# Kernel optimization log

Measured on AMD Instinct MI355X. Metric: run time of the kernel, lower is better.

The kernel has to match this reference:

```python
import jax, jax.numpy as jnp
import numpy as np

N = 1024
ODE_UNFOLDS = 6
EPS = 1e-8
RICCATI_ITERS = 6  # fixed-point DARE iteration standing in for the (undefined) lqr() helper
MASK_DENSITY = 0.4


def lqr(A, B, Q, R):
    # Discrete-time Riccati iteration: P <- A'PA - A'PB (R+B'PB)^{-1} B'PA + Q
    P = Q
    for _ in range(RICCATI_ITERS):
        BtP = B.T @ P                         # [N,N]
        K = jnp.linalg.solve(R + BtP @ B, BtP @ A)
        P = A.T @ P @ (A - B @ K) + Q
    BtP = B.T @ P
    K = jnp.linalg.solve(R + BtP @ B, BtP @ A)
    return K, P


def setup_inputs() -> dict:
    key = jax.random.key(0)
    ks = jax.random.split(key, 24)
    u = lambda k, shape, lo, hi: jax.random.uniform(k, shape, jnp.float32, lo, hi)
    # sprandsym-style SPD laplacian param, rescaled to [0.001, 1]
    rng = np.random.default_rng(0)
    X = (rng.standard_normal((N, N)) * (rng.random((N, N)) < 0.1)).astype(np.float32)
    A = X @ X.T + 0.01 * np.eye(N, dtype=np.float32)
    A = (A - A.min()) / (A.max() - A.min())
    lap = (A * (1.0 - 0.001) + 0.001).astype(np.float32)

    mask = (jax.random.uniform(ks[2], (N, N)) < MASK_DENSITY).astype(jnp.float32)
    smask = (jax.random.uniform(ks[3], (N, N)) < MASK_DENSITY).astype(jnp.float32)
    return dict(
        inputs=jax.random.normal(ks[0], (N,), jnp.float32),
        adj=jax.random.uniform(ks[1], (N, N), jnp.float32) / N,  # scaled for numerical stability of the Riccati loop
        laplacian=jnp.asarray(lap),
        control=u(ks[6], (N,), 0.001, 4.0),
        gleak=u(ks[7], (N,), 0.001, 1.0),
        vleak=u(ks[8], (N,), -0.2, 0.2),
        cm=u(ks[9], (N,), 0.4, 0.6),
        sigma=u(ks[10], (N, N), 3.0, 8.0),
        mu=u(ks[11], (N, N), 0.3, 0.8),
        w=u(ks[12], (N, N), 0.001, 1.0),
        erev=jnp.sign(jax.random.normal(ks[4], (N, N))) * mask,
        sensory_sigma=u(ks[13], (N, N), 3.0, 8.0),
        sensory_mu=u(ks[14], (N, N), 0.3, 0.8),
        sensory_w=u(ks[15], (N, N), 0.001, 1.0),
        sensory_erev=jnp.sign(jax.random.normal(ks[5], (N, N))) * smask,
        sparsity_mask=mask,
        sensory_sparsity_mask=smask,
        input_w=jnp.ones((N,), jnp.float32),
        input_b=jnp.zeros((N,), jnp.float32),
        output_w=jnp.ones((N,), jnp.float32),
        output_b=jnp.zeros((N,), jnp.float32),
        attn_w=jax.random.normal(ks[16], (N,), jnp.float32) / jnp.sqrt(N),
        attn_b=jax.random.normal(ks[17], (1,), jnp.float32),
        gc_w=jax.random.normal(ks[18], (1, 1), jnp.float32),
        gc_b=jax.random.normal(ks[19], (1,), jnp.float32),
    )


def reference(inputs, adj, laplacian, control, gleak, vleak, cm, sigma, mu, w, erev,
              sensory_sigma, sensory_mu, sensory_w, sensory_erev,
              sparsity_mask, sensory_sparsity_mask,
              input_w, input_b, output_w, output_b, attn_w, attn_b, gc_w, gc_b):
    x = inputs * input_w + input_b                      # _map_inputs (affine)
    n = x.shape[0]

    # ControlAttention with R = Q = eye(N): fc(I) rows = attn_w + attn_b
    att = attn_w + attn_b[0]                            # [N]
    s = x * att
    att_e = jnp.exp(s - jnp.max(s))                     # stable exp weighting
    Qm = jnp.diag(att_e)
    Rm = jnp.diag(att_e)                                # Q_att == R_att since Q == R == I

    K, _ = lqr(adj, laplacian, Qm, Rm)                  # K: [N,N]
    ctrl = (control - jnp.mean(K * x, axis=1)) @ laplacian  # [N]

    # sensory synapse activation (constant over the unfold loop)
    sens_act = sensory_w * jax.nn.sigmoid(sensory_sigma * (x[:, None] - sensory_mu)) * sensory_sparsity_mask
    w_num_s = jnp.sum(sens_act * sensory_erev, axis=1)  # [N]
    w_den_s = jnp.sum(sens_act, axis=1)                 # [N]

    gcn = lambda h: jax.nn.relu(adj @ (h * gc_w[0, 0]) + gc_b[0])
    d = x[:, None]
    for _ in range(4):
        d = gcn(d)
    d = d[:, 0]

    cm_t = d + cm * ODE_UNFOLDS + ctrl                  # elapsed_time = 1.0 -> cm / (1/unfolds)

    v = jnp.zeros((n,), x.dtype)                        # states default: zeros
    for _ in range(ODE_UNFOLDS):
        w_act = w * jax.nn.sigmoid(sigma * (v[:, None] - mu)) * sparsity_mask
        w_num = jnp.sum(w_act * erev, axis=1) + w_num_s
        w_den = jnp.sum(w_act, axis=1) + w_den_s
        v = (cm_t * v + gleak * vleak + w_num) / (cm_t + gleak + w_den + EPS)

    out = v * output_w + output_b                       # motor_size == state_size path
    return out, v, laplacian, ctrl + control
```

## Files before the change

### kernel.cpp

```cpp
#include <hip/hip_runtime.h>

#define MSZ (1024*1024)
#define LD 1024


__global__ __launch_bounds__(1024) void prep_k(const float* __restrict__ inp, const float* __restrict__ iw,
    const float* __restrict__ ib, const float* __restrict__ aw, const float* __restrict__ ab,
    float* __restrict__ xv, float* __restrict__ atte) {
  __shared__ float red[1024];
  int t = threadIdx.x;
  float x = inp[t] * iw[t] + ib[t];
  float s = x * (aw[t] + ab[0]);
  xv[t] = x;
  red[t] = s;
  __syncthreads();
  for (int o = 512; o > 0; o >>= 1) { if (t < o) red[t] = fmaxf(red[t], red[t + o]); __syncthreads(); }
  atte[t] = expf(s - red[0]);
}

__global__ void setdiag_k(float* __restrict__ P, const float* __restrict__ atte) {
  int idx = blockIdx.x * 256 + threadIdx.x;
  int r = idx >> 10, c = idx & 1023;
  P[idx] = (r == c) ? atte[r] : 0.0f;
}

__global__ __launch_bounds__(256) void sens_k(const float* __restrict__ sw, const float* __restrict__ ssig,
    const float* __restrict__ smu, const float* __restrict__ serev, const float* __restrict__ smask,
    const float* __restrict__ xv, float* __restrict__ wns, float* __restrict__ wds) {
  __shared__ float rn[256], rd[256];
  int i = blockIdx.x, t = threadIdx.x;
  float xi = xv[i];
  float n = 0.f, d = 0.f;
  for (int j = t; j < 1024; j += 256) {
    int idx = i * 1024 + j;
    float z = ssig[idx] * (xi - smu[idx]);
    float sg = 1.0f / (1.0f + expf(-z));
    float act = sw[idx] * sg * smask[idx];
    n += act * serev[idx];
    d += act;
  }
  rn[t] = n; rd[t] = d;
  __syncthreads();
  for (int o = 128; o > 0; o >>= 1) { if (t < o) { rn[t] += rn[t + o]; rd[t] += rd[t + o]; } __syncthreads(); }
  if (t == 0) { wns[i] = rn[0]; wds[i] = rd[0]; }
}

__global__ __launch_bounds__(256) void gcn_k(const float* __restrict__ adj, const float* __restrict__ hin,
    float* __restrict__ hout, const float* __restrict__ gcw, const float* __restrict__ gcb) {
  __shared__ float red[256];
  int i = blockIdx.x, t = threadIdx.x;
  float s = 0.f;
  for (int j = t; j < 1024; j += 256) s += adj[(size_t)i * 1024 + j] * hin[j];
  red[t] = s; __syncthreads();
  for (int o = 128; o > 0; o >>= 1) { if (t < o) red[t] += red[t + o]; __syncthreads(); }
  if (t == 0) hout[i] = fmaxf(gcw[0] * red[0] + gcb[0], 0.0f);
}

__global__ __launch_bounds__(256) void matvec_n_k(const float* __restrict__ M, const float* __restrict__ v,
    float* __restrict__ out) {
  __shared__ float red[256];
  int i = blockIdx.x, t = threadIdx.x;
  float s = 0.f;
  for (int j = t; j < 1024; j += 256) s += M[(size_t)i * 1024 + j] * v[j];
  red[t] = s; __syncthreads();
  for (int o = 128; o > 0; o >>= 1) { if (t < o) red[t] += red[t + o]; __syncthreads(); }
  if (t == 0) out[i] = red[0];
}

__global__ __launch_bounds__(256) void matvec_t_k(const float* __restrict__ M, const float* __restrict__ v,
    float* __restrict__ out) {
  int j = blockIdx.x * 256 + threadIdx.x;
  float s = 0.f;
  for (int i = 0; i < 1024; i++) s += M[(size_t)i * 1024 + j] * v[i];
  out[j] = s;
}

__global__ void gctrl_k(const float* __restrict__ control, const float* __restrict__ u, float* __restrict__ g) {
  int t = blockIdx.x * 256 + threadIdx.x;
  g[t] = control[t] - u[t] * (1.0f / 1024.0f);
}

__global__ void copylap_k(const float4* __restrict__ src, float4* __restrict__ dst) {
  int i = blockIdx.x * 256 + threadIdx.x;
  dst[i] = src[i];
}


struct GDesc { const float* A; const float* B; float* C; const float* diag; int tri; int mode; };
struct GArgs { GDesc d[3]; };

template<int TA>
__global__ __launch_bounds__(256) void gemm64x128_k(GArgs ga) {
  GDesc de = ga.d[blockIdx.z];
  int row0 = blockIdx.y * 64, col0 = blockIdx.x * 128;
  if (de.tri && row0 + 64 <= col0) return;
  __shared__ float As[32][64];
  __shared__ float Bs[32][128];
  const float* __restrict__ A = de.A;
  const float* __restrict__ B = de.B;
  int t = threadIdx.x;
  int tx = t & 15, ty = t >> 4;
  float acc[4][8] = {};
  for (int k0 = 0; k0 < 1024; k0 += 32) {
    if (TA == 1) {
      #pragma unroll
      for (int h = 0; h < 2; h++) {
        int s = h * 256 + t;
        int bk = s >> 4, am = (s & 15) * 4;
        float4 v = *(const float4*)(A + (size_t)(k0 + bk) * LD + row0 + am);
        *(float4*)(&As[bk][am]) = v;
      }
    } else {
      #pragma unroll
      for (int h = 0; h < 2; h++) {
        int s = h * 256 + t;
        int am = s >> 3, k4 = (s & 7) * 4;
        float4 v = *(const float4*)(A + (size_t)(row0 + am) * LD + k0 + k4);
        As[k4 + 0][am] = v.x; As[k4 + 1][am] = v.y; As[k4 + 2][am] = v.z; As[k4 + 3][am] = v.w;
      }
    }
    #pragma unroll
    for (int h = 0; h < 4; h++) {
      int s = h * 256 + t;
      int bk = s >> 5, bn = (s & 31) * 4;
      float4 v = *(const float4*)(B + (size_t)(k0 + bk) * LD + col0 + bn);
      *(float4*)(&Bs[bk][bn]) = v;
    }
    __syncthreads();
    #pragma unroll
    for (int k = 0; k < 32; k++) {
      float4 a4 = *(float4*)(&As[k][tx * 4]);
      float4 b0 = *(float4*)(&Bs[k][ty * 8]);
      float4 b1 = *(float4*)(&Bs[k][ty * 8 + 4]);
      float a[4] = {a4.x, a4.y, a4.z, a4.w};
      float b[8] = {b0.x, b0.y, b0.z, b0.w, b1.x, b1.y, b1.z, b1.w};
      #pragma unroll
      for (int i = 0; i < 4; i++)
        #pragma unroll
        for (int j = 0; j < 8; j++)
          acc[i][j] += a[i] * b[j];
    }
    __syncthreads();
  }
  #pragma unroll
  for (int i = 0; i < 4; i++) {
    int gm = row0 + tx * 4 + i;
    if (de.diag) {
      int dc = gm - col0 - ty * 8;
      if (dc >= 0 && dc < 8) acc[i][dc] += de.diag[gm];
    }
    float* cp = de.C + (size_t)gm * LD + col0 + ty * 8;
    if (de.mode == 0) {
      float4 o0 = {acc[i][0], acc[i][1], acc[i][2], acc[i][3]};
      float4 o1 = {acc[i][4], acc[i][5], acc[i][6], acc[i][7]};
      *(float4*)cp = o0; *(float4*)(cp + 4) = o1;
    } else {
      float4 c0 = *(float4*)cp, c1 = *(float4*)(cp + 4);
      c0.x -= acc[i][0]; c0.y -= acc[i][1]; c0.z -= acc[i][2]; c0.w -= acc[i][3];
      c1.x -= acc[i][4]; c1.y -= acc[i][5]; c1.z -= acc[i][6]; c1.w -= acc[i][7];
      *(float4*)cp = c0; *(float4*)(cp + 4) = c1;
    }
  }
}


__device__ __forceinline__ void potf2_wave(const float* Mg, int e, int l, float r[64]) {
  #pragma unroll
  for (int k = 0; k < 64; k++) r[k] = Mg[(size_t)(e + l) * LD + e + k];
  #pragma unroll
  for (int j = 0; j < 64; j++) {
    float dj = __shfl(r[j], j, 64);
    float Ljj = sqrtf(fmaxf(dj, 1e-12f));
    float inv = 1.0f / Ljj;
    if (l == j) r[j] = Ljj;
    else if (l > j) r[j] *= inv;
    #pragma unroll
    for (int k = j + 1; k < 64; k++) {
      float Lkj = __shfl(r[j], k, 64);
      r[k] -= r[j] * Lkj;
    }
  }
}

__global__ __launch_bounds__(256) void cpr_k(const float* __restrict__ Mm, float* __restrict__ Lb,
    float* __restrict__ S, int e, int nPanel) {
  __shared__ float L11s[64][65];
  int t = threadIdx.x;
  if (t < 64) {
    float r[64];
    potf2_wave(Mm, e, t, r);
    #pragma unroll
    for (int k = 0; k < 64; k++) if (k <= t) L11s[t][k] = r[k];
    if (blockIdx.x == 0) {
      #pragma unroll
      for (int k = 0; k < 64; k++) if (k <= t) Lb[(size_t)(e + t) * LD + e + k] = r[k];
    }
  }
  __syncthreads();
  if ((int)blockIdx.x < nPanel) {
    int row = e + 64 + blockIdx.x * 256 + t;
    if (row < 1024) {
      float y[64];
      #pragma unroll
      for (int k = 0; k < 64; k++) y[k] = Mm[(size_t)row * LD + e + k];
      #pragma unroll
      for (int kk = 0; kk < 64; kk++) {
        float v = y[kk];
        #pragma unroll
        for (int m = 0; m < kk; m++) v -= L11s[kk][m] * y[m];
        y[kk] = v / L11s[kk][kk];
      }
      #pragma unroll
      for (int k = 0; k < 64; k++) Lb[(size_t)row * LD + e + k] = y[k];
    }
  } else if (S) {
    int col = ((int)blockIdx.x - nPanel) * 256 + t;
    float y[64];
    #pragma unroll
    for (int k = 0; k < 64; k++) y[k] = S[(size_t)(e + k) * LD + col];
    #pragma unroll
    for (int kk = 0; kk < 64; kk++) {
      float v = y[kk];
      #pragma unroll
      for (int m = 0; m < kk; m++) v -= L11s[kk][m] * y[m];
      y[kk] = v / L11s[kk][kk];
    }
    #pragma unroll
    for (int k = 0; k < 64; k++) S[(size_t)(e + k) * LD + col] = y[k];
  }
}

__global__ __launch_bounds__(256) void chupd_k(const float* __restrict__ Lb, float* __restrict__ Mm,
    float* __restrict__ S, int e, int nSyrk) {
  __shared__ float As[32][64];
  __shared__ float Bs[32][128];
  int e2 = e + 64;
  int t = threadIdx.x;
  int tx = t & 15, ty = t >> 4;
  int bid = blockIdx.x;
  if (bid < nSyrk) {
    int ti = (int)((sqrtf(8.0f * bid + 1.0f) - 1.0f) * 0.5f);
    while ((ti + 1) * (ti + 2) / 2 <= bid) ti++;
    while (ti * (ti + 1) / 2 > bid) ti--;
    int tj = bid - ti * (ti + 1) / 2;
    int ra = e2 + ti * 64, rbb = e2 + tj * 64;
    float acc[4][4] = {};
    for (int k0 = 0; k0 < 64; k0 += 32) {
      #pragma unroll
      for (int h = 0; h < 2; h++) {
        int s = h * 256 + t;
        int r = s >> 3, k4 = (s & 7) * 4;
        float4 v = *(const float4*)(Lb + (size_t)(ra + r) * LD + e + k0 + k4);
        As[k4 + 0][r] = v.x; As[k4 + 1][r] = v.y; As[k4 + 2][r] = v.z; As[k4 + 3][r] = v.w;
        float4 u = *(const float4*)(Lb + (size_t)(rbb + r) * LD + e + k0 + k4);
        Bs[k4 + 0][r] = u.x; Bs[k4 + 1][r] = u.y; Bs[k4 + 2][r] = u.z; Bs[k4 + 3][r] = u.w;
      }
      __syncthreads();
      #pragma unroll
      for (int k = 0; k < 32; k++) {
        float4 a4 = *(float4*)(&As[k][tx * 4]);
        float4 b4 = *(float4*)(&Bs[k][ty * 4]);
        float a[4] = {a4.x, a4.y, a4.z, a4.w};
        float b[4] = {b4.x, b4.y, b4.z, b4.w};
        #pragma unroll
        for (int i = 0; i < 4; i++)
          #pragma unroll
          for (int j = 0; j < 4; j++)
            acc[i][j] += a[i] * b[j];
      }
      __syncthreads();
    }
    #pragma unroll
    for (int i = 0; i < 4; i++) {
      float* cp = Mm + (size_t)(ra + tx * 4 + i) * LD + rbb + ty * 4;
      float4 c = *(float4*)cp;
      c.x -= acc[i][0]; c.y -= acc[i][1]; c.z -= acc[i][2]; c.w -= acc[i][3];
      *(float4*)cp = c;
    }
  } else {
    int q = bid - nSyrk;
    int ti = q >> 3, cb = q & 7;
    int ra = e2 + ti * 64, c0 = cb * 128;
    float acc[4][8] = {};
    for (int k0 = 0; k0 < 64; k0 += 32) {
      #pragma unroll
      for (int h = 0; h < 2; h++) {
        int s = h * 256 + t;
        int r = s >> 3, k4 = (s & 7) * 4;
        float4 v = *(const float4*)(Lb + (size_t)(ra + r) * LD + e + k0 + k4);
        As[k4 + 0][r] = v.x; As[k4 + 1][r] = v.y; As[k4 + 2][r] = v.z; As[k4 + 3][r] = v.w;
      }
      #pragma unroll
      for (int h = 0; h < 4; h++) {
        int s = h * 256 + t;
        int bk = s >> 5, c4 = (s & 31) * 4;
        float4 v = *(const float4*)(S + (size_t)(e + k0 + bk) * LD + c0 + c4);
        *(float4*)(&Bs[bk][c4]) = v;
      }
      __syncthreads();
      #pragma unroll
      for (int k = 0; k < 32; k++) {
        float4 a4 = *(float4*)(&As[k][tx * 4]);
        float4 b0 = *(float4*)(&Bs[k][ty * 8]);
        float4 b1 = *(float4*)(&Bs[k][ty * 8 + 4]);
        float a[4] = {a4.x, a4.y, a4.z, a4.w};
        float b[8] = {b0.x, b0.y, b0.z, b0.w, b1.x, b1.y, b1.z, b1.w};
        #pragma unroll
        for (int i = 0; i < 4; i++)
          #pragma unroll
          for (int j = 0; j < 8; j++)
            acc[i][j] += a[i] * b[j];
      }
      __syncthreads();
    }
    #pragma unroll
    for (int i = 0; i < 4; i++) {
      float* cp = S + (size_t)(ra + tx * 4 + i) * LD + c0 + ty * 8;
      float4 c0v = *(float4*)cp, c1v = *(float4*)(cp + 4);
      c0v.x -= acc[i][0]; c0v.y -= acc[i][1]; c0v.z -= acc[i][2]; c0v.w -= acc[i][3];
      c1v.x -= acc[i][4]; c1v.y -= acc[i][5]; c1v.z -= acc[i][6]; c1v.w -= acc[i][7];
      *(float4*)cp = c0v; *(float4*)(cp + 4) = c1v;
    }
  }
}

__global__ __launch_bounds__(256) void mirror_k(float* __restrict__ P, const float* __restrict__ atte) {
  __shared__ float tile[64][65];
  int b = blockIdx.x, t = threadIdx.x;
  int ti, tj;
  if (b < 16) { ti = b; tj = b; }
  else {
    int p = b - 16;
    ti = (int)((1.0f + sqrtf(1.0f + 8.0f * p)) * 0.5f);
    while (ti * (ti - 1) / 2 > p) ti--;
    while ((ti + 1) * ti / 2 <= p) ti++;
    tj = p - ti * (ti - 1) / 2;
  }
  #pragma unroll
  for (int h = 0; h < 4; h++) {
    int s = h * 256 + t;
    int r = s >> 4, c4 = (s & 15) * 4;
    *(float4*)(&tile[r][c4]) = *(const float4*)(P + (size_t)(ti * 64 + r) * LD + tj * 64 + c4);
  }
  __syncthreads();
  if (ti == tj) {
    #pragma unroll
    for (int h = 0; h < 4; h++) {
      int s = h * 256 + t;
      int r = s >> 4, c4 = (s & 15) * 4;
      #pragma unroll
      for (int j = 0; j < 4; j++) {
        int c = c4 + j;
        if (c > r) P[(size_t)(ti * 64 + r) * LD + tj * 64 + c] = tile[c][r];
        else if (c == r) P[(size_t)(ti * 64 + r) * LD + tj * 64 + c] = tile[r][r] + atte[ti * 64 + r];
      }
    }
  } else {
    #pragma unroll
    for (int h = 0; h < 4; h++) {
      int s = h * 256 + t;
      int r = s >> 4, c4 = (s & 15) * 4;
      float4 o = {tile[c4 + 0][r], tile[c4 + 1][r], tile[c4 + 2][r], tile[c4 + 3][r]};
      *(float4*)(P + (size_t)(tj * 64 + r) * LD + ti * 64 + c4) = o;
    }
  }
}


__global__ __launch_bounds__(1024) void trsv_fwd_k(const float* __restrict__ Lg, const float* __restrict__ bin,
    float* __restrict__ wout) {
  __shared__ float zs[1024];
  __shared__ float wsb[64];
  int t = threadIdx.x;
  zs[t] = bin[t];
  __syncthreads();
  for (int s = 0; s < 16; s++) {
    int e = s * 64;
    if (t < 64) {
      float rr[64];
      #pragma unroll
      for (int k = 0; k < 64; k++) rr[k] = Lg[(size_t)(e + t) * LD + e + k];
      float acc = zs[e + t];
      #pragma unroll
      for (int k = 0; k < 64; k++) {
        float cand = acc / rr[k];
        float wk = __shfl(cand, k, 64);
        if (t == k) wsb[k] = wk;
        if (t > k) acc -= rr[k] * wk;
      }
    }
    __syncthreads();
    if (t < 64) zs[e + t] = wsb[t];
    __syncthreads();
    if (t >= e + 64) {
      float a = zs[t];
      #pragma unroll
      for (int k = 0; k < 64; k++) a -= Lg[(size_t)t * LD + e + k] * wsb[k];
      zs[t] = a;
    }
    __syncthreads();
  }
  wout[t] = zs[t];
}

__global__ __launch_bounds__(1024) void trsv_bwd_k(const float* __restrict__ Lg, const float* __restrict__ bin,
    float* __restrict__ wout) {
  __shared__ float zs[1024];
  __shared__ float wsb[64];
  int t = threadIdx.x;
  zs[t] = bin[t];
  __syncthreads();
  for (int s = 15; s >= 0; s--) {
    int e = s * 64;
    if (t < 64) {
      float rr[64];
      #pragma unroll
      for (int k = 0; k < 64; k++) rr[k] = Lg[(size_t)(e + k) * LD + e + t];
      float acc = zs[e + t];
      #pragma unroll
      for (int k = 63; k >= 0; k--) {
        float cand = acc / rr[k];
        float wk = __shfl(cand, k, 64);
        if (t == k) wsb[k] = wk;
        if (t < k) acc -= rr[k] * wk;
      }
    }
    __syncthreads();
    if (t < 64) zs[e + t] = wsb[t];
    __syncthreads();
    if (t < e) {
      float a = zs[t];
      #pragma unroll
      for (int k = 0; k < 64; k++) a -= Lg[(size_t)(e + k) * LD + t] * wsb[k];
      zs[t] = a;
    }
    __syncthreads();
  }
  wout[t] = zs[t];
}

__global__ __launch_bounds__(256) void ode_k(const float* __restrict__ w, const float* __restrict__ sig,
    const float* __restrict__ mu, const float* __restrict__ erev, const float* __restrict__ mask,
    const float* __restrict__ gleak, const float* __restrict__ vleak, const float* __restrict__ cm,
    const float* __restrict__ dvec, const float* __restrict__ ctrlv, const float* __restrict__ wns,
    const float* __restrict__ wds, const float* __restrict__ ow, const float* __restrict__ ob,
    const float* __restrict__ control, float* __restrict__ dout) {
  __shared__ float wm[1024], we[1024], sgs[1024], mus[1024];
  __shared__ float red[512];
  __shared__ float vsh;
  int i = blockIdx.x, t = threadIdx.x;
  for (int j = t; j < 1024; j += 256) {
    int idx = i * 1024 + j;
    float wmv = w[idx] * mask[idx];
    wm[j] = wmv;
    we[j] = wmv * erev[idx];
    sgs[j] = sig[idx];
    mus[j] = mu[idx];
  }
  float cmt = dvec[i] + cm[i] * 6.0f + ctrlv[i];
  float gl = gleak[i], vl = vleak[i];
  float numS = wns[i], denS = wds[i];
  float v = 0.0f;
  __syncthreads();
  for (int u = 0; u < 6; u++) {
    float n = 0.f, d = 0.f;
    for (int j = t; j < 1024; j += 256) {
      float sgm = 1.0f / (1.0f + expf(-sgs[j] * (v - mus[j])));
      n += we[j] * sgm;
      d += wm[j] * sgm;
    }
    red[t] = n; red[256 + t] = d;
    __syncthreads();
    for (int o = 128; o > 0; o >>= 1) {
      if (t < o) { red[t] += red[t + o]; red[256 + t] += red[256 + t + o]; }
      __syncthreads();
    }
    if (t == 0) {
      float num = red[0] + numS, den = red[256] + denS;
      vsh = (cmt * v + gl * vl + num) / (cmt + gl + den + 1e-8f);
    }
    __syncthreads();
    v = vsh;
    __syncthreads();
  }
  if (t == 0) {
    dout[i] = v * ow[i] + ob[i];
    dout[1024 + i] = v;
    dout[2048 + 1048576 + i] = ctrlv[i] + control[i];
  }
}


static void launch_chol_tri(const float* Mm, float* Lb, float* S, hipStream_t stream) {
  for (int s = 0; s < 16; s++) {
    int e = s * 64;
    int rb = 1024 - e - 64;
    int nPanel = (rb + 255) / 256;
    int nRhs = S ? 4 : 0;
    int nBlocks = nPanel + nRhs; if (nBlocks < 1) nBlocks = 1;
    cpr_k<<<nBlocks, 256, 0, stream>>>(Mm, Lb, S, e, nPanel);
    if (rb > 0) {
      int nt = rb / 64;
      int nSyrk = nt * (nt + 1) / 2;
      int nUpd = nSyrk + (S ? nt * 8 : 0);
      chupd_k<<<nUpd, 256, 0, stream>>>(Lb, (float*)Mm, S, e, nSyrk);
    }
  }
}

extern "C" void kernel_launch(void* const* d_in, const int* in_sizes, int n_in,
                              void* d_out, int out_size, void* d_ws, size_t ws_size,
                              hipStream_t stream) {
  const float* inputs  = (const float*)d_in[0];
  const float* adj     = (const float*)d_in[1];
  const float* lap     = (const float*)d_in[2];
  const float* control = (const float*)d_in[3];
  const float* gleak   = (const float*)d_in[4];
  const float* vleak   = (const float*)d_in[5];
  const float* cm      = (const float*)d_in[6];
  const float* sigma   = (const float*)d_in[7];
  const float* mu      = (const float*)d_in[8];
  const float* w       = (const float*)d_in[9];
  const float* erev    = (const float*)d_in[10];
  const float* ssig    = (const float*)d_in[11];
  const float* smu     = (const float*)d_in[12];
  const float* sw      = (const float*)d_in[13];
  const float* serev   = (const float*)d_in[14];
  const float* mask    = (const float*)d_in[15];
  const float* smask   = (const float*)d_in[16];
  const float* iw      = (const float*)d_in[17];
  const float* ib      = (const float*)d_in[18];
  const float* ow      = (const float*)d_in[19];
  const float* ob      = (const float*)d_in[20];
  const float* aw      = (const float*)d_in[21];
  const float* ab      = (const float*)d_in[22];
  const float* gcw     = (const float*)d_in[23];
  const float* gcb     = (const float*)d_in[24];
  float* out = (float*)d_out;
  float* ws = (float*)d_ws;

  float* P0 = ws;
  float* P1 = ws + (size_t)MSZ;
  float* PA = ws + 2 * (size_t)MSZ;
  float* PB = ws + 3 * (size_t)MSZ;
  float* Mm = ws + 4 * (size_t)MSZ;
  float* S  = ws + 5 * (size_t)MSZ;
  float* vb = ws + 6 * (size_t)MSZ;
  float* xv = vb;            float* atte = vb + 1024;
  float* wns = vb + 2048;    float* wds  = vb + 3072;
  float* dA  = vb + 4096;    float* dB   = vb + 5120;
  float* yv  = vb + 6144;    float* tv   = vb + 7168;
  float* zv  = vb + 8192;    float* wv   = vb + 9216;
  float* uv  = vb + 10240;   float* gv   = vb + 11264;
  float* ctrlv = vb + 12288;

  prep_k<<<1, 1024, 0, stream>>>(inputs, iw, ib, aw, ab, xv, atte);
  setdiag_k<<<4096, 256, 0, stream>>>(P0, atte);
  sens_k<<<1024, 256, 0, stream>>>(sw, ssig, smu, serev, smask, xv, wns, wds);
  gcn_k<<<1024, 256, 0, stream>>>(adj, xv, dA, gcw, gcb);
  gcn_k<<<1024, 256, 0, stream>>>(adj, dA, dB, gcw, gcb);
  gcn_k<<<1024, 256, 0, stream>>>(adj, dB, dA, gcw, gcb);
  gcn_k<<<1024, 256, 0, stream>>>(adj, dA, dB, gcw, gcb);

  float* P = P0; float* Pn = P1;
  for (int it = 0; it < 6; it++) {
    GArgs g1 = {{ {P, adj, PA, nullptr, 0, 0}, {P, lap, PB, nullptr, 0, 0}, {nullptr,nullptr,nullptr,nullptr,0,0} }};
    gemm64x128_k<0><<<dim3(8, 16, 2), 256, 0, stream>>>(g1);
    GArgs g2 = {{ {PB, adj, S, nullptr, 0, 0}, {PB, lap, Mm, atte, 1, 0}, {adj, PA, Pn, nullptr, 1, 0} }};
    gemm64x128_k<1><<<dim3(8, 16, 3), 256, 0, stream>>>(g2);
    launch_chol_tri(Mm, PA, S, stream);
    GArgs g3 = {{ {S, S, Pn, nullptr, 1, 1}, {nullptr,nullptr,nullptr,nullptr,0,0}, {nullptr,nullptr,nullptr,nullptr,0,0} }};
    gemm64x128_k<1><<<dim3(8, 16, 1), 256, 0, stream>>>(g3);
    mirror_k<<<136, 256, 0, stream>>>(Pn, atte);
    float* tmp = P; P = Pn; Pn = tmp;
  }

  GArgs g4 = {{ {P, lap, PB, nullptr, 0, 0}, {nullptr,nullptr,nullptr,nullptr,0,0}, {nullptr,nullptr,nullptr,nullptr,0,0} }};
  gemm64x128_k<0><<<dim3(8, 16, 1), 256, 0, stream>>>(g4);
  GArgs g5 = {{ {PB, lap, Mm, atte, 1, 0}, {nullptr,nullptr,nullptr,nullptr,0,0}, {nullptr,nullptr,nullptr,nullptr,0,0} }};
  gemm64x128_k<1><<<dim3(8, 16, 1), 256, 0, stream>>>(g5);
  launch_chol_tri(Mm, PA, nullptr, stream);
  matvec_n_k<<<1024, 256, 0, stream>>>(adj, xv, yv);
  matvec_n_k<<<1024, 256, 0, stream>>>(P, yv, tv);
  matvec_t_k<<<4, 256, 0, stream>>>(lap, tv, zv);
  trsv_fwd_k<<<1, 1024, 0, stream>>>(PA, zv, wv);
  trsv_bwd_k<<<1, 1024, 0, stream>>>(PA, wv, uv);
  gctrl_k<<<4, 256, 0, stream>>>(control, uv, gv);
  matvec_t_k<<<4, 256, 0, stream>>>(lap, gv, ctrlv);

  ode_k<<<1024, 256, 0, stream>>>(w, sigma, mu, erev, mask, gleak, vleak, cm, dB, ctrlv,
                                  wns, wds, ow, ob, control, out);
  copylap_k<<<1024, 256, 0, stream>>>((const float4*)lap, (float4*)(out + 2048));
}
```

Baseline: 15.65 ms.

## Fuse blocked Cholesky and triangular solve into one persistent kernel with grid barriers

```diff
diff --git a/kernel.cpp b/kernel.cpp
--- a/kernel.cpp
+++ b/kernel.cpp
@@ -71,6 +71,7 @@
     float* __restrict__ out) {
   int j = blockIdx.x * 256 + threadIdx.x;
   float s = 0.f;
+  #pragma unroll 8
   for (int i = 0; i < 1024; i++) s += M[(size_t)i * 1024 + j] * v[i];
   out[j] = s;
 }
@@ -164,9 +165,28 @@
 }
 
 
-__device__ __forceinline__ void potf2_wave(const float* Mg, int e, int l, float r[64]) {
+__device__ __forceinline__ void gsync(int* bar) {
+  __syncthreads();
+  if (threadIdx.x == 0) {
+    __threadfence();
+    int gen = __hip_atomic_load(bar + 1, __ATOMIC_RELAXED, __HIP_MEMORY_SCOPE_AGENT);
+    int n = __hip_atomic_fetch_add(bar, 1, __ATOMIC_ACQ_REL, __HIP_MEMORY_SCOPE_AGENT);
+    if (n + 1 == (int)gridDim.x) {
+      __hip_atomic_store(bar, 0, __ATOMIC_RELAXED, __HIP_MEMORY_SCOPE_AGENT);
+      __hip_atomic_store(bar + 1, gen + 1, __ATOMIC_RELEASE, __HIP_MEMORY_SCOPE_AGENT);
+    } else {
+      while (__hip_atomic_load(bar + 1, __ATOMIC_ACQUIRE, __HIP_MEMORY_SCOPE_AGENT) == gen) {
+        __builtin_amdgcn_s_sleep(1);
+      }
+    }
+    __threadfence();
+  }
+  __syncthreads();
+}
+
+__device__ __forceinline__ void potf2_lds(float (*T)[132], int l, float r[64]) {
   #pragma unroll
-  for (int k = 0; k < 64; k++) r[k] = Mg[(size_t)(e + l) * LD + e + k];
+  for (int k = 0; k < 64; k++) r[k] = T[l][k];
   #pragma unroll
   for (int j = 0; j < 64; j++) {
     float dj = __shfl(r[j], j, 64);
@@ -182,145 +202,184 @@
   }
 }
 
-__global__ __launch_bounds__(256) void cpr_k(const float* __restrict__ Mm, float* __restrict__ Lb,
-    float* __restrict__ S, int e, int nPanel) {
-  __shared__ float L11s[64][65];
+__global__ __launch_bounds__(256) void cfs_k(float* __restrict__ Mm, float* __restrict__ Lb,
+                                             float* __restrict__ S, int* __restrict__ bar) {
+  __shared__ float shA[64][68];
+  __shared__ float shB[64][132];
   int t = threadIdx.x;
-  if (t < 64) {
-    float r[64];
-    potf2_wave(Mm, e, t, r);
+  int bid = blockIdx.x;
+  int nb = gridDim.x;
+
+  if (bid == 0) {
     #pragma unroll
-    for (int k = 0; k < 64; k++) if (k <= t) L11s[t][k] = r[k];
-    if (blockIdx.x == 0) {
-      #pragma unroll
-      for (int k = 0; k < 64; k++) if (k <= t) Lb[(size_t)(e + t) * LD + e + k] = r[k];
-    }
-  }
-  __syncthreads();
-  if ((int)blockIdx.x < nPanel) {
-    int row = e + 64 + blockIdx.x * 256 + t;
-    if (row < 1024) {
-      float y[64];
-      #pragma unroll
-      for (int k = 0; k < 64; k++) y[k] = Mm[(size_t)row * LD + e + k];
-      #pragma unroll
-      for (int kk = 0; kk < 64; kk++) {
-        float v = y[kk];
+    for (int h = 0; h < 4; h++) {
+      int q = h * 256 + t, r = q >> 4, c4 = (q & 15) * 4;
+      *(float4*)(&shB[r][c4]) = *(const float4*)(Mm + (size_t)r * LD + c4);
+    }
+    __syncthreads();
+    if (t < 64) {
+      float r[64];
+      potf2_lds(shB, t, r);
+      #pragma unroll
+      for (int k = 0; k < 64; k++) if (k <= t) Lb[(size_t)t * LD + k] = r[k];
+    }
+  }
+  gsync(bar);
+
+  for (int s = 0; s < 16; s++) {
+    int e = s * 64, e2 = e + 64, nt = 15 - s, rb = nt * 64;
+    int nPanel = (rb + 255) / 256;
+    int nRhs = S ? 4 : 0;
+    int njA = nPanel + nRhs;
+    if (bid < njA) {
+      #pragma unroll
+      for (int h = 0; h < 4; h++) {
+        int q = h * 256 + t, r = q >> 4, c4 = (q & 15) * 4;
+        *(float4*)(&shA[r][c4]) = *(const float4*)(Lb + (size_t)(e + r) * LD + e + c4);
+      }
+      __syncthreads();
+      if (bid < nPanel) {
+        int row = e2 + bid * 256 + t;
+        if (row < 1024) {
+          float y[64];
+          #pragma unroll
+          for (int k = 0; k < 64; k++) y[k] = Mm[(size_t)row * LD + e + k];
+          #pragma unroll
+          for (int kk = 0; kk < 64; kk++) {
+            float v = y[kk];
+            #pragma unroll
+            for (int m = 0; m < kk; m++) v -= shA[kk][m] * y[m];
+            y[kk] = v / shA[kk][kk];
+          }
+          #pragma unroll
+          for (int k = 0; k < 64; k++) Lb[(size_t)row * LD + e + k] = y[k];
+        }
+      } else {
+        int col = (bid - nPanel) * 256 + t;
+        float y[64];
         #pragma unroll
-        for (int m = 0; m < kk; m++) v -= L11s[kk][m] * y[m];
-        y[kk] = v / L11s[kk][kk];
-      }
-      #pragma unroll
-      for (int k = 0; k < 64; k++) Lb[(size_t)row * LD + e + k] = y[k];
-    }
-  } else if (S) {
-    int col = ((int)blockIdx.x - nPanel) * 256 + t;
-    float y[64];
-    #pragma unroll
-    for (int k = 0; k < 64; k++) y[k] = S[(size_t)(e + k) * LD + col];
-    #pragma unroll
-    for (int kk = 0; kk < 64; kk++) {
-      float v = y[kk];
-      #pragma unroll
-      for (int m = 0; m < kk; m++) v -= L11s[kk][m] * y[m];
-      y[kk] = v / L11s[kk][kk];
-    }
-    #pragma unroll
-    for (int k = 0; k < 64; k++) S[(size_t)(e + k) * LD + col] = y[k];
-  }
-}
-
-__global__ __launch_bounds__(256) void chupd_k(const float* __restrict__ Lb, float* __restrict__ Mm,
-    float* __restrict__ S, int e, int nSyrk) {
-  __shared__ float As[32][64];
-  __shared__ float Bs[32][128];
-  int e2 = e + 64;
-  int t = threadIdx.x;
-  int tx = t & 15, ty = t >> 4;
-  int bid = blockIdx.x;
-  if (bid < nSyrk) {
-    int ti = (int)((sqrtf(8.0f * bid + 1.0f) - 1.0f) * 0.5f);
-    while ((ti + 1) * (ti + 2) / 2 <= bid) ti++;
-    while (ti * (ti + 1) / 2 > bid) ti--;
-    int tj = bid - ti * (ti + 1) / 2;
-    int ra = e2 + ti * 64, rbb = e2 + tj * 64;
-    float acc[4][4] = {};
-    for (int k0 = 0; k0 < 64; k0 += 32) {
-      #pragma unroll
-      for (int h = 0; h < 2; h++) {
-        int s = h * 256 + t;
-        int r = s >> 3, k4 = (s & 7) * 4;
-        float4 v = *(const float4*)(Lb + (size_t)(ra + r) * LD + e + k0 + k4);
-        As[k4 + 0][r] = v.x; As[k4 + 1][r] = v.y; As[k4 + 2][r] = v.z; As[k4 + 3][r] = v.w;
-        float4 u = *(const float4*)(Lb + (size_t)(rbb + r) * LD + e + k0 + k4);
-        Bs[k4 + 0][r] = u.x; Bs[k4 + 1][r] = u.y; Bs[k4 + 2][r] = u.z; Bs[k4 + 3][r] = u.w;
-      }
-      __syncthreads();
-      #pragma unroll
-      for (int k = 0; k < 32; k++) {
-        float4 a4 = *(float4*)(&As[k][tx * 4]);
-        float4 b4 = *(float4*)(&Bs[k][ty * 4]);
-        float a[4] = {a4.x, a4.y, a4.z, a4.w};
-        float b[4] = {b4.x, b4.y, b4.z, b4.w};
+        for (int k = 0; k < 64; k++) y[k] = S[(size_t)(e + k) * LD + col];
         #pragma unroll
-        for (int i = 0; i < 4; i++)
+        for (int kk = 0; kk < 64; kk++) {
+          float v = y[kk];
           #pragma unroll
-          for (int j = 0; j < 4; j++)
-            acc[i][j] += a[i] * b[j];
-      }
-      __syncthreads();
-    }
-    #pragma unroll
-    for (int i = 0; i < 4; i++) {
-      float* cp = Mm + (size_t)(ra + tx * 4 + i) * LD + rbb + ty * 4;
-      float4 c = *(float4*)cp;
-      c.x -= acc[i][0]; c.y -= acc[i][1]; c.z -= acc[i][2]; c.w -= acc[i][3];
-      *(float4*)cp = c;
-    }
-  } else {
-    int q = bid - nSyrk;
-    int ti = q >> 3, cb = q & 7;
-    int ra = e2 + ti * 64, c0 = cb * 128;
-    float acc[4][8] = {};
-    for (int k0 = 0; k0 < 64; k0 += 32) {
-      #pragma unroll
-      for (int h = 0; h < 2; h++) {
-        int s = h * 256 + t;
-        int r = s >> 3, k4 = (s & 7) * 4;
-        float4 v = *(const float4*)(Lb + (size_t)(ra + r) * LD + e + k0 + k4);
-        As[k4 + 0][r] = v.x; As[k4 + 1][r] = v.y; As[k4 + 2][r] = v.z; As[k4 + 3][r] = v.w;
-      }
-      #pragma unroll
-      for (int h = 0; h < 4; h++) {
-        int s = h * 256 + t;
-        int bk = s >> 5, c4 = (s & 31) * 4;
-        float4 v = *(const float4*)(S + (size_t)(e + k0 + bk) * LD + c0 + c4);
-        *(float4*)(&Bs[bk][c4]) = v;
-      }
-      __syncthreads();
-      #pragma unroll
-      for (int k = 0; k < 32; k++) {
-        float4 a4 = *(float4*)(&As[k][tx * 4]);
-        float4 b0 = *(float4*)(&Bs[k][ty * 8]);
-        float4 b1 = *(float4*)(&Bs[k][ty * 8 + 4]);
-        float a[4] = {a4.x, a4.y, a4.z, a4.w};
-        float b[8] = {b0.x, b0.y, b0.z, b0.w, b1.x, b1.y, b1.z, b1.w};
+          for (int m = 0; m < kk; m++) v -= shA[kk][m] * y[m];
+          y[kk] = v / shA[kk][kk];
+        }
         #pragma unroll
-        for (int i = 0; i < 4; i++)
+        for (int k = 0; k < 64; k++) S[(size_t)(e + k) * LD + col] = y[k];
+      }
+    }
+    gsync(bar);
+    if (nt > 0) {
+      if (bid == 0) {
+        #pragma unroll
+        for (int h = 0; h < 4; h++) {
+          int q = h * 256 + t, r = q >> 4, c4 = (q & 15) * 4;
+          *(float4*)(&shA[r][c4]) = *(const float4*)(Lb + (size_t)(e2 + r) * LD + e + c4);
+        }
+        __syncthreads();
+        for (int idx = t; idx < 4096; idx += 256) {
+          int r = idx >> 6, c = idx & 63;
+          float a = Mm[(size_t)(e2 + r) * LD + e2 + c];
           #pragma unroll
-          for (int j = 0; j < 8; j++)
-            acc[i][j] += a[i] * b[j];
-      }
-      __syncthreads();
-    }
-    #pragma unroll
-    for (int i = 0; i < 4; i++) {
-      float* cp = S + (size_t)(ra + tx * 4 + i) * LD + c0 + ty * 8;
-      float4 c0v = *(float4*)cp, c1v = *(float4*)(cp + 4);
-      c0v.x -= acc[i][0]; c0v.y -= acc[i][1]; c0v.z -= acc[i][2]; c0v.w -= acc[i][3];
-      c1v.x -= acc[i][4]; c1v.y -= acc[i][5]; c1v.z -= acc[i][6]; c1v.w -= acc[i][7];
-      *(float4*)cp = c0v; *(float4*)(cp + 4) = c1v;
-    }
+          for (int k = 0; k < 64; k++) a -= shA[r][k] * shA[c][k];
+          shB[r][c] = a;
+        }
+        __syncthreads();
+        if (t < 64) {
+          float r[64];
+          potf2_lds(shB, t, r);
+          #pragma unroll
+          for (int k = 0; k < 64; k++) if (k <= t) Lb[(size_t)(e2 + t) * LD + e2 + k] = r[k];
+        }
+      } else {
+        int nSyrk = nt * (nt + 1) / 2 - 1;
+        int nSupd = S ? nt * 8 : 0;
+        int njB = nSyrk + nSupd;
+        for (int job = bid - 1; job < njB; job += nb - 1) {
+          if (job < nSyrk) {
+            int q = job + 1;
+            int i0 = (int)((sqrtf(8.0f * q + 1.0f) - 1.0f) * 0.5f);
+            while ((i0 + 1) * (i0 + 2) / 2 <= q) i0++;
+            while (i0 * (i0 + 1) / 2 > q) i0--;
+            int j0 = q - i0 * (i0 + 1) / 2;
+            int ra = e + 64 * (i0 + 1), rc = e + 64 * (j0 + 1);
+            #pragma unroll
+            for (int h = 0; h < 4; h++) {
+              int qq = h * 256 + t, r = qq >> 4, c4 = (qq & 15) * 4;
+              *(float4*)(&shA[r][c4]) = *(const float4*)(Lb + (size_t)(ra + r) * LD + e + c4);
+              *(float4*)(&shB[r][c4]) = *(const float4*)(Lb + (size_t)(rc + r) * LD + e + c4);
+            }
+            __syncthreads();
+            int tx = t & 15, ty = t >> 4;
+            float acc[4][4] = {};
+            #pragma unroll 8
+            for (int k = 0; k < 64; k++) {
+              float a[4], b[4];
+              #pragma unroll
+              for (int i = 0; i < 4; i++) a[i] = shA[tx * 4 + i][k];
+              #pragma unroll
+              for (int j = 0; j < 4; j++) b[j] = shB[ty * 4 + j][k];
+              #pragma unroll
+              for (int i = 0; i < 4; i++)
+                #pragma unroll
+                for (int j = 0; j < 4; j++)
+                  acc[i][j] += a[i] * b[j];
+            }
+            #pragma unroll
+            for (int i = 0; i < 4; i++) {
+              float* cp = Mm + (size_t)(ra + tx * 4 + i) * LD + rc + ty * 4;
+              float4 c = *(float4*)cp;
+              c.x -= acc[i][0]; c.y -= acc[i][1]; c.z -= acc[i][2]; c.w -= acc[i][3];
+              *(float4*)cp = c;
+            }
+            __syncthreads();
+          } else {
+            int q = job - nSyrk;
+            int i0 = (q >> 3) + 1, cb = q & 7;
+            int ra = e + 64 * i0, c0 = cb * 128;
+            #pragma unroll
+            for (int h = 0; h < 4; h++) {
+              int qq = h * 256 + t, r = qq >> 4, c4 = (qq & 15) * 4;
+              *(float4*)(&shA[r][c4]) = *(const float4*)(Lb + (size_t)(ra + r) * LD + e + c4);
+            }
+            #pragma unroll
+            for (int h = 0; h < 8; h++) {
+              int qq = h * 256 + t, r = qq >> 5, c4 = (qq & 31) * 4;
+              *(float4*)(&shB[r][c4]) = *(const float4*)(S + (size_t)(e + r) * LD + c0 + c4);
+            }
+            __syncthreads();
+            int tx = t & 15, ty = t >> 4;
+            float acc[4][8] = {};
+            #pragma unroll 8
+            for (int k = 0; k < 64; k++) {
+              float a[4];
+              #pragma unroll
+              for (int i = 0; i < 4; i++) a[i] = shA[tx * 4 + i][k];
+              float4 b0 = *(float4*)(&shB[k][ty * 8]);
+              float4 b1 = *(float4*)(&shB[k][ty * 8 + 4]);
+              float b[8] = {b0.x, b0.y, b0.z, b0.w, b1.x, b1.y, b1.z, b1.w};
+              #pragma unroll
+              for (int i = 0; i < 4; i++)
+                #pragma unroll
+                for (int j = 0; j < 8; j++)
+                  acc[i][j] += a[i] * b[j];
+            }
+            #pragma unroll
+            for (int i = 0; i < 4; i++) {
+              float* cp = S + (size_t)(ra + tx * 4 + i) * LD + c0 + ty * 8;
+              float4 v0 = *(float4*)cp, v1 = *(float4*)(cp + 4);
+              v0.x -= acc[i][0]; v0.y -= acc[i][1]; v0.z -= acc[i][2]; v0.w -= acc[i][3];
+              v1.x -= acc[i][4]; v1.y -= acc[i][5]; v1.z -= acc[i][6]; v1.w -= acc[i][7];
+              *(float4*)cp = v0; *(float4*)(cp + 4) = v1;
+            }
+            __syncthreads();
+          }
+        }
+      }
+    }
+    gsync(bar);
   }
 }
 
@@ -490,23 +549,6 @@
   }
 }
 
-
-static void launch_chol_tri(const float* Mm, float* Lb, float* S, hipStream_t stream) {
-  for (int s = 0; s < 16; s++) {
-    int e = s * 64;
-    int rb = 1024 - e - 64;
-    int nPanel = (rb + 255) / 256;
-    int nRhs = S ? 4 : 0;
-    int nBlocks = nPanel + nRhs; if (nBlocks < 1) nBlocks = 1;
-    cpr_k<<<nBlocks, 256, 0, stream>>>(Mm, Lb, S, e, nPanel);
-    if (rb > 0) {
-      int nt = rb / 64;
-      int nSyrk = nt * (nt + 1) / 2;
-      int nUpd = nSyrk + (S ? nt * 8 : 0);
-      chupd_k<<<nUpd, 256, 0, stream>>>(Lb, (float*)Mm, S, e, nSyrk);
-    }
-  }
-}
 
 extern "C" void kernel_launch(void* const* d_in, const int* in_sizes, int n_in,
                               void* d_out, int out_size, void* d_ws, size_t ws_size,
@@ -553,6 +595,9 @@
   float* zv  = vb + 8192;    float* wv   = vb + 9216;
   float* uv  = vb + 10240;   float* gv   = vb + 11264;
   float* ctrlv = vb + 12288;
+  int*   bar = (int*)(vb + 16384);
+
+  hipMemsetAsync(bar, 0, 2 * sizeof(int), stream);
 
   prep_k<<<1, 1024, 0, stream>>>(inputs, iw, ib, aw, ab, xv, atte);
   setdiag_k<<<4096, 256, 0, stream>>>(P0, atte);
@@ -568,7 +613,7 @@
     gemm64x128_k<0><<<dim3(8, 16, 2), 256, 0, stream>>>(g1);
     GArgs g2 = {{ {PB, adj, S, nullptr, 0, 0}, {PB, lap, Mm, atte, 1, 0}, {adj, PA, Pn, nullptr, 1, 0} }};
     gemm64x128_k<1><<<dim3(8, 16, 3), 256, 0, stream>>>(g2);
-    launch_chol_tri(Mm, PA, S, stream);
+    cfs_k<<<256, 256, 0, stream>>>(Mm, PA, S, bar);
     GArgs g3 = {{ {S, S, Pn, nullptr, 1, 1}, {nullptr,nullptr,nullptr,nullptr,0,0}, {nullptr,nullptr,nullptr,nullptr,0,0} }};
     gemm64x128_k<1><<<dim3(8, 16, 1), 256, 0, stream>>>(g3);
     mirror_k<<<136, 256, 0, stream>>>(Pn, atte);
@@ -579,7 +624,7 @@
   gemm64x128_k<0><<<dim3(8, 16, 1), 256, 0, stream>>>(g4);
   GArgs g5 = {{ {PB, lap, Mm, atte, 1, 0}, {nullptr,nullptr,nullptr,nullptr,0,0}, {nullptr,nullptr,nullptr,nullptr,0,0} }};
   gemm64x128_k<1><<<dim3(8, 16, 1), 256, 0, stream>>>(g5);
-  launch_chol_tri(Mm, PA, nullptr, stream);
+  cfs_k<<<256, 256, 0, stream>>>(Mm, PA, nullptr, bar);
   matvec_n_k<<<1024, 256, 0, stream>>>(adj, xv, yv);
   matvec_n_k<<<1024, 256, 0, stream>>>(P, yv, tv);
   matvec_t_k<<<4, 256, 0, stream>>>(lap, tv, zv);
```

Measured after the change: 44.42 ms. +183.8%, slower.
